# Optimization experiments

Measured on AMD Instinct MI355X. Metric: run time of the kernel, lower is better.

Reference implementation:

```python
import jax, jax.numpy as jnp
import numpy as np
from jax import lax

B = 32768
INPUT_SIZE = 42  # 1 rocket_y + 20*(rock_x, rock_y) + 1 speed
H, W = 10, 15    # grid_height, grid_width
OUT = 3


def setup_inputs() -> dict:
    key = jax.random.key(0)
    ks = jax.random.split(key, 8)
    p = lambda k, s: (jax.random.normal(k, s) * 0.05).astype(jnp.float32)
    x = (jax.random.uniform(ks[0], (B, INPUT_SIZE)) * 16.0).astype(jnp.float32)
    return {
        "x": x,
        "conv1_w": p(ks[1], (16, 2, 3, 3)), "conv1_b": jnp.zeros((16,), jnp.float32),
        "conv2_w": p(ks[2], (32, 16, 3, 3)), "conv2_b": jnp.zeros((32,), jnp.float32),
        "fc1_w": p(ks[3], (32 * H * W + 1, 256)), "fc1_b": jnp.zeros((256,), jnp.float32),
        "fc2_w": p(ks[4], (256, 128)), "fc2_b": jnp.zeros((128,), jnp.float32),
        "fc3_w": p(ks[5], (128, OUT)), "fc3_b": jnp.zeros((OUT,), jnp.float32),
    }


def _conv(h, w, b):
    # 3x3, stride 1, padding 1 (SAME), NCHW / OIHW
    return lax.conv_general_dilated(h, w, (1, 1), "SAME",
                                    dimension_numbers=("NCHW", "OIHW", "NCHW")) \
           + b[None, :, None, None]


def _build_grid(x):
    """Vectorized replacement of the per-sample Python scatter loop."""
    bsz = x.shape[0]
    b = jnp.arange(bsz)
    dt = x.dtype
    # rocket channel: grid[i, rocket_y, 1] = 1 if 0 <= rocket_y < H
    ry = x[:, 0].astype(jnp.int32)
    rv = ((ry >= 0) & (ry < H)).astype(dt)
    rocket = jnp.zeros((bsz, H, W), dt).at[b, jnp.clip(ry, 0, H - 1), 1].add(rv)
    # rock channel: pairs (x, y) at columns (1,2),(3,4),...,(39,40)
    kx = x[:, 1:INPUT_SIZE - 1:2].astype(jnp.int32)  # [B, 20]
    ky = x[:, 2:INPUT_SIZE - 1:2].astype(jnp.int32)  # [B, 20]
    kv = ((kx >= 0) & (ky >= 0) & (kx < W) & (ky < H)).astype(dt)
    rock = jnp.zeros((bsz, H, W), dt).at[
        b[:, None], jnp.clip(ky, 0, H - 1), jnp.clip(kx, 0, W - 1)
    ].max(kv)  # set-to-1 semantics (duplicates ok)
    return jnp.stack([rocket, rock], axis=1)  # [B, 2, H, W]


def reference(x, conv1_w, conv1_b, conv2_w, conv2_b,
              fc1_w, fc1_b, fc2_w, fc2_b, fc3_w, fc3_b):
    grid = _build_grid(x)
    h = jax.nn.relu(_conv(grid, conv1_w, conv1_b))
    h = jax.nn.relu(_conv(h, conv2_w, conv2_b))
    h = h.reshape(x.shape[0], -1)                      # NCHW flatten, matches torch .view
    h = jnp.concatenate([h, x[:, -1:]], axis=1)        # append speed
    h = jax.nn.relu(h @ fc1_w + fc1_b)
    h = jax.nn.relu(h @ fc2_w + fc2_b)
    return h @ fc3_w + fc3_b
```

## Files before the change

### kernel.cpp

```cpp
#include <hip/hip_runtime.h>
#include <hip/hip_bf16.h>
#include <stdint.h>

typedef short short8 __attribute__((ext_vector_type(8)));
typedef float f32x4  __attribute__((ext_vector_type(4)));

__device__ __forceinline__ uint16_t f2bf(float f) {
    union { float f; uint32_t u; } v; v.f = f;
    return (uint16_t)((v.u + 0x7FFFu + ((v.u >> 16) & 1u)) >> 16);
}
__device__ __forceinline__ float bf2f(uint16_t h) {
    union { uint32_t u; float f; } v; v.u = ((uint32_t)h) << 16;
    return v.f;
}
__device__ __forceinline__ void gl_lds16(const void* g, void* l) {
    __builtin_amdgcn_global_load_lds(
        (const __attribute__((address_space(1))) unsigned int*)g,
        (__attribute__((address_space(3))) unsigned int*)l, 16, 0, 0);
}

#define NSAMP_TOT 32768
#define H2_PER_S  5120

__global__ void repack_all(const float* __restrict__ f1w, const float* __restrict__ c2w,
                           const float* __restrict__ c1w, const float* __restrict__ f2w,
                           uint16_t* __restrict__ w1pt, uint16_t* __restrict__ w2rt,
                           uint16_t* __restrict__ w1rt, uint16_t* __restrict__ w2bt) {
    int tid = threadIdx.x, b = blockIdx.x;
    if (b < 160) {
        int f_s = b >> 4, cp = b & 15, n = tid;
        __align__(16) uint16_t vals[32];
        #pragma unroll
        for (int o = 0; o < 32; o++) {
            int c = cp * 2 + (o >> 4), pl = o & 15;
            int p = f_s * 16 + pl;
            float v = (p < 150) ? f1w[(size_t)(c * 150 + p) * 256 + n] : 0.f;
            vals[o] = f2bf(v);
        }
        int win = f_s * 8 + (cp >> 1);
        size_t rowbase = (size_t)n * H2_PER_S + win * 64;
        #pragma unroll
        for (int j = 0; j < 4; j++) {
            int qlog = (cp * 4 + j) & 7;
            int qphy = qlog ^ (n & 7);
            *(uint4*)&w1pt[rowbase + qphy * 8] = *(uint4*)&vals[j * 8];
        }
    } else if (b == 160) {
        for (int t = tid; t < 32 * 160; t += 256) {
            int n = t / 160, k = t % 160;
            float v = 0.f;
            if (k < 144) {
                int tap = k >> 4, ci = k & 15, dy = tap / 3, dx = tap % 3;
                v = c2w[((n * 16 + ci) * 3 + dy) * 3 + dx];
            }
            w2rt[t] = f2bf(v);
        }
        for (int t = tid; t < 16 * 32; t += 256) {
            int n = t >> 5, k = t & 31;
            float v = 0.f;
            if (k < 18) {
                int tap = k >> 1, ch = k & 1;
                int dy = (tap * 11) >> 5, dx = tap - dy * 3;
                v = c1w[((n * 2 + ch) * 3 + dy) * 3 + dx];
            }
            w1rt[t] = f2bf(v);
        }
    } else {
        __shared__ float tr2[32][129];
        int kb = b - 161;
        for (int i = tid; i < 32 * 128; i += 256) {
            int kk = i >> 7, n = i & 127;
            tr2[kk][n] = f2w[(size_t)(kb * 32 + kk) * 128 + n];
        }
        __syncthreads();
        int n = tid >> 1, half = tid & 1;
        __align__(16) uint16_t tmp[16];
        #pragma unroll
        for (int q = 0; q < 16; q++) tmp[q] = f2bf(tr2[half * 16 + q][n]);
        *(uint4*)&w2bt[(size_t)n * 256 + kb * 32 + half * 16]     = *(uint4*)&tmp[0];
        *(uint4*)&w2bt[(size_t)n * 256 + kb * 32 + half * 16 + 8] = *(uint4*)&tmp[8];
    }
}

__launch_bounds__(512, 2)
__global__ void k12_fused(const float* __restrict__ x, const uint16_t* __restrict__ w1rt,
                          const float* __restrict__ c1b, const uint16_t* __restrict__ w2rt,
                          const float* __restrict__ c2b, uint16_t* __restrict__ h2, int s0) {
    __shared__ float sx[8 * 42];
    __shared__ __align__(16) uint16_t grd[8 * 204 * 2];
    __shared__ __align__(16) uint16_t h1s[8 * 204 * 16];
    int tid = threadIdx.x;
    int w = tid >> 6, l = tid & 63, lr = l & 15, lk = l >> 4;

    short8 b1f = *(const short8*)&w1rt[lr * 32 + lk * 8];
    short8 bfr[5][2];
    #pragma unroll
    for (int ks = 0; ks < 5; ks++)
        #pragma unroll
        for (int nf = 0; nf < 2; nf++)
            bfr[ks][nf] = *(const short8*)&w2rt[(nf * 16 + lr) * 160 + ks * 32 + lk * 8];
    float cb1r = c1b[lr];
    float cb0 = c2b[lr], cb1 = c2b[16 + lr];

    uint4 z4 = make_uint4(0, 0, 0, 0);
    for (int i = tid; i < 3672; i += 512) {
        if (i < 408) ((uint4*)grd)[i] = z4;
        else         ((uint4*)h1s)[i - 408] = z4;
    }
    int sbase = s0 + blockIdx.x * 8;
    for (int i = tid; i < 8 * 42; i += 512) sx[i] = x[(size_t)(sbase + i / 42) * 42 + (i % 42)];
    __syncthreads();

    if (tid < 160) {
        int sl = tid / 20, r = tid % 20;
        int kx = (int)sx[sl * 42 + 1 + 2 * r];
        int ky = (int)sx[sl * 42 + 2 + 2 * r];
        if (kx >= 0 && kx < 15 && ky >= 0 && ky < 10)
            grd[(sl * 204 + (ky + 1) * 17 + (kx + 1)) * 2 + 1] = 0x3F80;
    } else if (tid < 168) {
        int sl = tid - 160;
        int ry = (int)sx[sl * 42];
        if (ry >= 0 && ry < 10)
            grd[(sl * 204 + (ry + 1) * 17 + 2) * 2 + 0] = 0x3F80;
    }
    __syncthreads();

    for (int f = w; f < 75; f += 8) {
        int rA = f * 16 + lr;
        int sA = rA / 150, pA = rA - sA * 150;
        int y = pA / 15, xx = pA - y * 15;
        int base = sA * 204 + y * 17 + xx;
        union { uint32_t d[4]; short8 s; } au;
        #pragma unroll
        for (int jj = 0; jj < 4; jj++) {
            int t = lk * 4 + jj;
            int valid = t < 9;
            int tc = valid ? t : 0;
            int dy = (tc * 11) >> 5, dx = tc - dy * 3;
            uint32_t v = *(const uint32_t*)&grd[(base + dy * 17 + dx) * 2];
            au.d[jj] = valid ? v : 0u;
        }
        f32x4 acc = {};
        acc = __builtin_amdgcn_mfma_f32_16x16x32_bf16(au.s, b1f, acc, 0, 0, 0);
        #pragma unroll
        for (int j = 0; j < 4; j++) {
            int row = f * 16 + lk * 4 + j;
            int s2 = row / 150, p2 = row - s2 * 150;
            int y2 = p2 / 15, x2 = p2 - y2 * 15;
            float v = acc[j] + cb1r;
            h1s[(s2 * 204 + (y2 + 1) * 17 + (x2 + 1)) * 16 + lr] = f2bf(v > 0.f ? v : 0.f);
        }
    }
    __syncthreads();

    short8 zz = {0, 0, 0, 0, 0, 0, 0, 0};
    for (int f = w; f < 80; f += 8) {
        int s_local = f / 10, f_s = f - s_local * 10;
        int p160 = f_s * 16 + lr;
        int pA = p160 < 150 ? p160 : 0;
        int y = pA / 15, xx = pA - y * 15;
        f32x4 acc0 = {}, acc1 = {};
        #pragma unroll
        for (int ks = 0; ks < 5; ks++) {
            int idx = ks * 4 + lk;
            int idc = idx < 18 ? idx : 0;
            int tap = idc >> 1, half = idc & 1;
            int dy = (tap * 11) >> 5, dx = tap - dy * 3;
            short8 av = *(const short8*)&h1s[((s_local * 204 + (y + dy) * 17 + (xx + dx)) * 16) + half * 8];
            av = idx < 18 ? av : zz;
            acc0 = __builtin_amdgcn_mfma_f32_16x16x32_bf16(av, bfr[ks][0], acc0, 0, 0, 0);
            acc1 = __builtin_amdgcn_mfma_f32_16x16x32_bf16(av, bfr[ks][1], acc1, 0, 0, 0);
        }
        ushort4 v0, v1;
        { float a = acc0[0] + cb0; v0.x = f2bf(a > 0.f ? a : 0.f); }
        { float a = acc0[1] + cb0; v0.y = f2bf(a > 0.f ? a : 0.f); }
        { float a = acc0[2] + cb0; v0.z = f2bf(a > 0.f ? a : 0.f); }
        { float a = acc0[3] + cb0; v0.w = f2bf(a > 0.f ? a : 0.f); }
        { float a = acc1[0] + cb1; v1.x = f2bf(a > 0.f ? a : 0.f); }
        { float a = acc1[1] + cb1; v1.y = f2bf(a > 0.f ? a : 0.f); }
        { float a = acc1[2] + cb1; v1.z = f2bf(a > 0.f ? a : 0.f); }
        { float a = acc1[3] + cb1; v1.w = f2bf(a > 0.f ? a : 0.f); }
        int k0 = f_s * 512 + lr * 16 + lk * 4;
        int k0s = (k0 & ~63) | (((((k0 >> 3) & 7) ^ s_local)) << 3) | (k0 & 7);
        int k1 = k0 + 256;
        int k1s = (k1 & ~63) | (((((k1 >> 3) & 7) ^ s_local)) << 3) | (k1 & 7);
        size_t sb = (size_t)(blockIdx.x * 8 + s_local) * H2_PER_S;
        *(ushort4*)&h2[sb + k0s] = v0;
        *(ushort4*)&h2[sb + k1s] = v1;
    }
}

__launch_bounds__(512)
__global__ void k3_fused(const uint16_t* __restrict__ h2, const uint16_t* __restrict__ w1pt,
                         const float* __restrict__ f1b, const float* __restrict__ f1w,
                         const float* __restrict__ x, const uint16_t* __restrict__ w2bt,
                         const float* __restrict__ f2b, const float* __restrict__ f3w,
                         const float* __restrict__ f3b, float* __restrict__ out, int s0) {
    #define BUF_E (64 * 64 + 256 * 64)
    __shared__ __align__(16) uint16_t uLDS[2 * BUF_E];
    uint16_t* lH = uLDS;
    __shared__ float sbias[256], swl[256], sspeed[64], sb2[128], sw3[384];
    __shared__ float pf[4][64][3];
    int tid = threadIdx.x;
    int bm = blockIdx.x;
    if (tid < 256) { sbias[tid] = f1b[tid]; swl[tid] = f1w[(size_t)4800 * 256 + tid]; }
    else if (tid < 320) sspeed[tid - 256] = x[(size_t)(s0 + bm * 64 + (tid - 256)) * 42 + 41];
    else if (tid < 448) sb2[tid - 320] = f2b[tid - 320];
    for (int i = tid; i < 384; i += 512) sw3[i] = f3w[i];

    int w = tid >> 6, l = tid & 63, lr = l & 15, lk = l >> 4;
    int wm = w >> 2, wn = w & 3;
    const uint16_t* ga = &h2[(size_t)(bm * 64 + (tid >> 3)) * H2_PER_S + (tid & 7) * 8];
    const uint16_t* gb[4];
    #pragma unroll
    for (int i = 0; i < 4; i++) {
        int c2 = tid + i * 512;
        gb[i] = &w1pt[(size_t)(c2 >> 3) * H2_PER_S + (c2 & 7) * 8];
    }
    uint16_t* laD[2]; uint16_t* lbD[2][4];
    #pragma unroll
    for (int bb = 0; bb < 2; bb++) {
        laD[bb] = uLDS + bb * BUF_E + tid * 8;
        #pragma unroll
        for (int i = 0; i < 4; i++)
            lbD[bb][i] = uLDS + bb * BUF_E + 4096 + (tid + i * 512) * 8;
    }
    int aoff[2][2], boff[4][2];
    #pragma unroll
    for (int ks = 0; ks < 2; ks++) {
        int cl = (ks * 4 + lk);
        #pragma unroll
        for (int mf = 0; mf < 2; mf++)
            aoff[mf][ks] = (wm * 32 + mf * 16 + lr) * 64 + ((cl ^ (lr & 7)) << 3);
        #pragma unroll
        for (int nf = 0; nf < 4; nf++)
            boff[nf][ks] = 4096 + (wn * 64 + nf * 16 + lr) * 64 + ((cl ^ (lr & 7)) << 3);
    }

    f32x4 acc[2][4] = {};
    gl_lds16(ga, laD[0]); ga += 64;
    #pragma unroll
    for (int i = 0; i < 4; i++) { gl_lds16(gb[i], lbD[0][i]); gb[i] += 64; }
    __syncthreads();
    for (int kt = 0; kt < 80; kt++) {
        int cur = kt & 1;
        if (kt < 79) {
            gl_lds16(ga, laD[cur ^ 1]); ga += 64;
            #pragma unroll
            for (int i = 0; i < 4; i++) { gl_lds16(gb[i], lbD[cur ^ 1][i]); gb[i] += 64; }
        }
        const uint16_t* buf = uLDS + cur * BUF_E;
        #pragma unroll
        for (int ks = 0; ks < 2; ks++) {
            short8 a[2], b[4];
            #pragma unroll
            for (int mf = 0; mf < 2; mf++)
                a[mf] = *(const short8*)&buf[aoff[mf][ks]];
            #pragma unroll
            for (int nf = 0; nf < 4; nf++)
                b[nf] = *(const short8*)&buf[boff[nf][ks]];
            #pragma unroll
            for (int mf = 0; mf < 2; mf++)
                #pragma unroll
                for (int nf = 0; nf < 4; nf++)
                    acc[mf][nf] = __builtin_amdgcn_mfma_f32_16x16x32_bf16(a[mf], b[nf], acc[mf][nf], 0, 0, 0);
        }
        __syncthreads();
    }
    #pragma unroll
    for (int mf = 0; mf < 2; mf++) {
        #pragma unroll
        for (int j = 0; j < 4; j++) {
            int r = wm * 32 + mf * 16 + lk * 4 + j;
            float sp = sspeed[r];
            #pragma unroll
            for (int nf = 0; nf < 4; nf++) {
                int col = wn * 64 + nf * 16 + lr;
                float v = acc[mf][nf][j] + sbias[col] + sp * swl[col];
                int cc = col >> 3, cl = col & 7;
                lH[r * 256 + ((cc ^ (r & 7)) << 3) + cl] = f2bf(v > 0.f ? v : 0.f);
            }
        }
    }
    __syncthreads();
    f32x4 acc2[2][2] = {};
    #pragma unroll
    for (int ks2 = 0; ks2 < 8; ks2++) {
        short8 a2[2], bv[2];
        #pragma unroll
        for (int mf2 = 0; mf2 < 2; mf2++) {
            int row = wm * 32 + mf2 * 16 + lr;
            int chunk = (ks2 * 4 + lk) ^ (row & 7);
            a2[mf2] = *(const short8*)&lH[row * 256 + chunk * 8];
        }
        #pragma unroll
        for (int nf2 = 0; nf2 < 2; nf2++)
            bv[nf2] = *(const short8*)&w2bt[(size_t)(wn * 32 + nf2 * 16 + lr) * 256 + ks2 * 32 + lk * 8];
        #pragma unroll
        for (int mf2 = 0; mf2 < 2; mf2++)
            #pragma unroll
            for (int nf2 = 0; nf2 < 2; nf2++)
                acc2[mf2][nf2] = __builtin_amdgcn_mfma_f32_16x16x32_bf16(a2[mf2], bv[nf2], acc2[mf2][nf2], 0, 0, 0);
    }
    float p3[2][4][3];
    #pragma unroll
    for (int mf2 = 0; mf2 < 2; mf2++)
        #pragma unroll
        for (int j = 0; j < 4; j++)
            #pragma unroll
            for (int o = 0; o < 3; o++) p3[mf2][j][o] = 0.f;
    #pragma unroll
    for (int mf2 = 0; mf2 < 2; mf2++) {
        #pragma unroll
        for (int nf2 = 0; nf2 < 2; nf2++) {
            int col = wn * 32 + nf2 * 16 + lr;
            float w0 = sw3[col * 3 + 0], w1v = sw3[col * 3 + 1], w2v = sw3[col * 3 + 2];
            #pragma unroll
            for (int j = 0; j < 4; j++) {
                float v = acc2[mf2][nf2][j] + sb2[col];
                v = v > 0.f ? v : 0.f;
                p3[mf2][j][0] += v * w0;
                p3[mf2][j][1] += v * w1v;
                p3[mf2][j][2] += v * w2v;
            }
        }
    }
    #pragma unroll
    for (int off = 1; off < 16; off <<= 1)
        #pragma unroll
        for (int mf2 = 0; mf2 < 2; mf2++)
            #pragma unroll
            for (int j = 0; j < 4; j++)
                #pragma unroll
                for (int o = 0; o < 3; o++)
                    p3[mf2][j][o] += __shfl_xor(p3[mf2][j][o], off);
    if (lr == 0) {
        #pragma unroll
        for (int mf2 = 0; mf2 < 2; mf2++)
            #pragma unroll
            for (int j = 0; j < 4; j++) {
                int r = wm * 32 + mf2 * 16 + lk * 4 + j;
                #pragma unroll
                for (int o = 0; o < 3; o++) pf[wn][r][o] = p3[mf2][j][o];
            }
    }
    __syncthreads();
    if (tid < 192) {
        int r = tid / 3, o = tid - r * 3;
        out[(size_t)(s0 + bm * 64 + r) * 3 + o] =
            pf[0][r][o] + pf[1][r][o] + pf[2][r][o] + pf[3][r][o] + f3b[o];
    }
    #undef BUF_E
}

extern "C" void kernel_launch(void* const* d_in, const int* in_sizes, int n_in,
                              void* d_out, int out_size, void* d_ws, size_t ws_size,
                              hipStream_t stream) {
    const float* x   = (const float*)d_in[0];
    const float* c1w = (const float*)d_in[1];
    const float* c1b = (const float*)d_in[2];
    const float* c2w = (const float*)d_in[3];
    const float* c2b = (const float*)d_in[4];
    const float* f1w = (const float*)d_in[5];
    const float* f1b = (const float*)d_in[6];
    const float* f2w = (const float*)d_in[7];
    const float* f2b = (const float*)d_in[8];
    const float* f3w = (const float*)d_in[9];
    const float* f3b = (const float*)d_in[10];
    float* out = (float*)d_out;

    char* ws = (char*)d_ws;
    uint16_t* w1pt = (uint16_t*)ws;
    uint16_t* w2rt = (uint16_t*)(ws + 2621440);
    uint16_t* w2bt = (uint16_t*)(ws + 2631680);
    uint16_t* w1rt = (uint16_t*)(ws + 2697216);
    size_t base = 2698240;

    int chunk = NSAMP_TOT;
    while (chunk > 128 && base + (size_t)chunk * 10240 > ws_size) chunk >>= 1;
    uint16_t* h2 = (uint16_t*)(ws + base);

    repack_all<<<169, 256, 0, stream>>>(f1w, c2w, c1w, f2w, w1pt, w2rt, w1rt, w2bt);

    for (int s0 = 0; s0 < NSAMP_TOT; s0 += chunk) {
        k12_fused<<<chunk / 8, 512, 0, stream>>>(x, w1rt, c1b, w2rt, c2b, h2, s0);
        k3_fused<<<chunk / 64, 512, 0, stream>>>(h2, w1pt, f1b, f1w, x, w2bt, f2b, f3w, f3b, out, s0);
    }
}
```

Before: 301.6 us.

## Triple-buffer fc1 GEMM LDS loads with explicit vmcnt waits and one barrier

Turns the fc1 GEMM main loop in k3_fused from double to triple buffering of LDS tiles filled by global_load_lds. Loads are issued two k-tiles ahead. Explicit s_waitcnt vmcnt counts replace the full __syncthreads, leaving a single s_barrier per iteration and rotating buffer pointers. The aim is to hide global load latency and cut synchronisation overhead. In exchange, LDS use rises to about 120KB per block. The new load into the rotating buffer is issued before the barrier, so a fast wave could overwrite a tile that slower waves are still reading.

Result: faster. 264.7 us (-12.2%).

```diff
diff --git a/kernel.cpp b/kernel.cpp
--- a/kernel.cpp
+++ b/kernel.cpp
@@ -197,7 +197,7 @@
                          const float* __restrict__ f2b, const float* __restrict__ f3w,
                          const float* __restrict__ f3b, float* __restrict__ out, int s0) {
     #define BUF_E (64 * 64 + 256 * 64)
-    __shared__ __align__(16) uint16_t uLDS[2 * BUF_E];
+    __shared__ __align__(16) uint16_t uLDS[3 * BUF_E];
     uint16_t* lH = uLDS;
     __shared__ float sbias[256], swl[256], sspeed[64], sb2[128], sw3[384];
     __shared__ float pf[4][64][3];
@@ -217,14 +217,10 @@
         int c2 = tid + i * 512;
         gb[i] = &w1pt[(size_t)(c2 >> 3) * H2_PER_S + (c2 & 7) * 8];
     }
-    uint16_t* laD[2]; uint16_t* lbD[2][4];
-    #pragma unroll
-    for (int bb = 0; bb < 2; bb++) {
-        laD[bb] = uLDS + bb * BUF_E + tid * 8;
-        #pragma unroll
-        for (int i = 0; i < 4; i++)
-            lbD[bb][i] = uLDS + bb * BUF_E + 4096 + (tid + i * 512) * 8;
-    }
+    int saOff = tid * 8;
+    int sbOff[4];
+    #pragma unroll
+    for (int i = 0; i < 4; i++) sbOff[i] = 4096 + (tid + i * 512) * 8;
     int aoff[2][2], boff[4][2];
     #pragma unroll
     for (int ks = 0; ks < 2; ks++) {
@@ -237,36 +233,49 @@
             boff[nf][ks] = 4096 + (wn * 64 + nf * 16 + lr) * 64 + ((cl ^ (lr & 7)) << 3);
     }
 
+    uint16_t* bufA = uLDS;
+    uint16_t* bufB = uLDS + BUF_E;
+    uint16_t* bufC = uLDS + 2 * BUF_E;
+
     f32x4 acc[2][4] = {};
-    gl_lds16(ga, laD[0]); ga += 64;
-    #pragma unroll
-    for (int i = 0; i < 4; i++) { gl_lds16(gb[i], lbD[0][i]); gb[i] += 64; }
-    __syncthreads();
+    gl_lds16(ga, bufA + saOff); ga += 64;
+    #pragma unroll
+    for (int i = 0; i < 4; i++) { gl_lds16(gb[i], bufA + sbOff[i]); gb[i] += 64; }
+    gl_lds16(ga, bufB + saOff); ga += 64;
+    #pragma unroll
+    for (int i = 0; i < 4; i++) { gl_lds16(gb[i], bufB + sbOff[i]); gb[i] += 64; }
+
     for (int kt = 0; kt < 80; kt++) {
-        int cur = kt & 1;
-        if (kt < 79) {
-            gl_lds16(ga, laD[cur ^ 1]); ga += 64;
-            #pragma unroll
-            for (int i = 0; i < 4; i++) { gl_lds16(gb[i], lbD[cur ^ 1][i]); gb[i] += 64; }
-        }
-        const uint16_t* buf = uLDS + cur * BUF_E;
+        if (kt < 78) {
+            gl_lds16(ga, bufC + saOff); ga += 64;
+            #pragma unroll
+            for (int i = 0; i < 4; i++) { gl_lds16(gb[i], bufC + sbOff[i]); gb[i] += 64; }
+            asm volatile("s_waitcnt vmcnt(10)" ::: "memory");
+        } else if (kt == 78) {
+            asm volatile("s_waitcnt vmcnt(5)" ::: "memory");
+        } else {
+            asm volatile("s_waitcnt vmcnt(0)" ::: "memory");
+        }
+        __builtin_amdgcn_s_barrier();
+        __builtin_amdgcn_sched_barrier(0);
         #pragma unroll
         for (int ks = 0; ks < 2; ks++) {
             short8 a[2], b[4];
             #pragma unroll
             for (int mf = 0; mf < 2; mf++)
-                a[mf] = *(const short8*)&buf[aoff[mf][ks]];
+                a[mf] = *(const short8*)&bufA[aoff[mf][ks]];
             #pragma unroll
             for (int nf = 0; nf < 4; nf++)
-                b[nf] = *(const short8*)&buf[boff[nf][ks]];
+                b[nf] = *(const short8*)&bufA[boff[nf][ks]];
             #pragma unroll
             for (int mf = 0; mf < 2; mf++)
                 #pragma unroll
                 for (int nf = 0; nf < 4; nf++)
                     acc[mf][nf] = __builtin_amdgcn_mfma_f32_16x16x32_bf16(a[mf], b[nf], acc[mf][nf], 0, 0, 0);
         }
-        __syncthreads();
-    }
+        uint16_t* t = bufA; bufA = bufB; bufB = bufC; bufC = t;
+    }
+    __syncthreads();
     #pragma unroll
     for (int mf = 0; mf < 2; mf++) {
         #pragma unroll
```
